# Performance work log

Hardware: AMD Instinct MI355X
Metric: run time of the kernel (lower is better)

## Reference

```python
import jax, jax.numpy as jnp
import numpy as np

N, K, C = 32768, 64, 256
PAIR, HID, BINS, CLIP = 32, 64, 16, 32
LN_EPS = 1e-5


def setup_inputs() -> dict:
    key = jax.random.key(0)
    ks = jax.random.split(key, 12)
    inp = {
        "features": jax.random.normal(ks[0], (N, C), jnp.float32),
        "resi": jnp.arange(N, dtype=jnp.int32),
        "chain": jax.random.randint(ks[1], (N,), 0, 4, jnp.int32),
        "batch": jax.random.randint(ks[2], (N,), 0, 8, jnp.int32),
        "neighbours": jax.random.randint(ks[3], (N, K), 0, N, jnp.int32),
        # learned params
        "W_left": jax.random.normal(ks[4], (C, PAIR), jnp.float32) / np.sqrt(C),
        "W_right": jax.random.normal(ks[5], (C, PAIR), jnp.float32) / np.sqrt(C),
        "W_pos": jax.random.normal(ks[6], (2 * CLIP + 1, PAIR), jnp.float32) * 0.1,
        "ln_scale": jnp.ones((PAIR,), jnp.float32),
        "ln_bias": jnp.zeros((PAIR,), jnp.float32),
        "W1": jax.random.normal(ks[7], (PAIR, HID), jnp.float32) / np.sqrt(PAIR),
        "b1": jnp.zeros((HID,), jnp.float32),
        "W2": jax.random.normal(ks[8], (HID, BINS), jnp.float32) / np.sqrt(HID),
        "b2": jnp.zeros((BINS,), jnp.float32),
    }
    return inp


def reference(features, resi, chain, batch, neighbours,
              W_left, W_right, W_pos, ln_scale, ln_bias, W1, b1, W2, b2):
    # left/right 32-dim codes, pairwise combine via neighbour gather: [N,K,32]
    left = features @ W_left
    right = features @ W_right
    dcode = left[:, None, :] + right[neighbours]

    # relative sequence position one-hot (65 classes) -> Linear(32, bias=False).
    # one_hot @ W_pos == row-gather of W_pos; masked to same chain & batch.
    rel = jnp.clip(resi[neighbours] - resi[:, None], -CLIP, CLIP) + CLIP  # [N,K]
    same = (chain[neighbours] == chain[:, None]) & (batch[neighbours] == batch[:, None])
    dcode = dcode + jnp.where(same[..., None], W_pos[rel], 0.0)

    # LayerNorm over last axis (scale + offset)
    mu = dcode.mean(-1, keepdims=True)
    var = jnp.mean(jnp.square(dcode - mu), -1, keepdims=True)
    dcode = (dcode - mu) * jax.lax.rsqrt(var + LN_EPS) * ln_scale + ln_bias

    # 2-layer GELU MLP -> 16 bins
    h = jax.nn.gelu(dcode @ W1 + b1)
    logits = h @ W2 + b2
    log_p = jax.nn.log_softmax(logits, axis=-1)

    # softmax-weighted expected distance over bin centers of [0, 22) A
    step = 22.0 / BINS
    bin_centers = (jnp.arange(BINS, dtype=jnp.float32) + 0.5) * step
    dmap = (jnp.exp(log_p) * bin_centers).sum(axis=-1)  # [N,K]
    return log_p, dmap
```

## Files before the change

### kernel.cpp

```cpp
#include <hip/hip_runtime.h>
#include <stdint.h>

#define N_RES 32768
#define KNEI  64
#define CFEAT 256
#define PAIRD 32
#define HIDD  64
#define NBINS 16
#define CLIPV 32
#define NGROUPS (N_RES * KNEI / 16)

typedef __attribute__((ext_vector_type(8))) short  short8;
typedef __attribute__((ext_vector_type(4))) float  float4_t;

union U8 { uint32_t u[4]; short8 s8; };

__device__ __forceinline__ uint32_t pkbf(float a, float b) {
    uint32_t ua = __float_as_uint(a) + 0x8000u;
    uint32_t ub = __float_as_uint(b) + 0x8000u;
    uint32_t d;
    const uint32_t sel = 0x07060302u;
    asm("v_perm_b32 %0, %1, %2, %3" : "=v"(d) : "v"(ub), "v"(ua), "s"(sel));
    return d;
}

__device__ __forceinline__ float fastrcp(float x) { return __builtin_amdgcn_rcpf(x); }
__device__ __forceinline__ float fexp2(float x)   { return __builtin_amdgcn_exp2f(x); }
__device__ __forceinline__ float flog2(float x)   { return __builtin_amdgcn_logf(x); }

__device__ __forceinline__ float gelu_tanh(float x) {
    const float k1 = 2.3022082f;
    const float k2 = 0.1029432f;
    float x2 = x * x;
    float t  = __builtin_fmaf(k2, x2, k1);
    float e  = fexp2(x * t);
    float th = __builtin_fmaf(-2.0f, fastrcp(e + 1.0f), 1.0f);
    float hx = 0.5f * x;
    return __builtin_fmaf(hx, th, hx);
}

__global__ __launch_bounds__(256) void proj_kernel(
    const float* __restrict__ feat, const float* __restrict__ Wl,
    const float* __restrict__ Wr, const int* __restrict__ resi,
    const int* __restrict__ chain, const int* __restrict__ batch,
    float* __restrict__ left, float* __restrict__ right,
    int4* __restrict__ meta)
{
    __shared__ __align__(16) float Wc[CFEAT * 64];
    const int tid = threadIdx.x;
    for (int idx = tid; idx < CFEAT * 32; idx += 256) {
        int k = idx >> 5, o = idx & 31;
        Wc[k * 64 + o]      = Wl[idx];
        Wc[k * 64 + 32 + o] = Wr[idx];
    }
    const int row_base = blockIdx.x * 64;
    if (meta != nullptr && tid < 64) {
        int r = row_base + tid;
        meta[r] = make_int4(resi[r], chain[r], batch[r], 0);
    }
    __syncthreads();

    const int cb = (tid & 7) * 8;
    const int r0 = row_base + (tid >> 3) * 2;

    float acc[2][8];
#pragma unroll
    for (int r = 0; r < 2; ++r)
#pragma unroll
        for (int j = 0; j < 8; ++j) acc[r][j] = 0.f;

    for (int i = 0; i < CFEAT; i += 4) {
        float4_t f0 = *(const float4_t*)(feat + (size_t)r0 * CFEAT + i);
        float4_t f1 = *(const float4_t*)(feat + (size_t)(r0 + 1) * CFEAT + i);
#pragma unroll
        for (int s = 0; s < 4; ++s) {
            float4_t wa = *(const float4_t*)(Wc + (i + s) * 64 + cb);
            float4_t wb = *(const float4_t*)(Wc + (i + s) * 64 + cb + 4);
#pragma unroll
            for (int j = 0; j < 4; ++j) {
                acc[0][j]     += f0[s] * wa[j];
                acc[0][4 + j] += f0[s] * wb[j];
                acc[1][j]     += f1[s] * wa[j];
                acc[1][4 + j] += f1[s] * wb[j];
            }
        }
    }
#pragma unroll
    for (int r = 0; r < 2; ++r) {
        float* dst = (cb < 32) ? (left  + (size_t)(r0 + r) * 32 + cb)
                               : (right + (size_t)(r0 + r) * 32 + (cb - 32));
        float4_t v0 = {acc[r][0], acc[r][1], acc[r][2], acc[r][3]};
        float4_t v1 = {acc[r][4], acc[r][5], acc[r][6], acc[r][7]};
        *(float4_t*)dst       = v0;
        *(float4_t*)(dst + 4) = v1;
    }
}

template <int USE_META>
__global__ __launch_bounds__(256, 8) void pair_kernel(
    const float* __restrict__ left, const float* __restrict__ right,
    const int* __restrict__ resi, const int* __restrict__ chain,
    const int* __restrict__ batch, const int* __restrict__ nbr,
    const int4* __restrict__ meta,
    const float* __restrict__ wpos, const float* __restrict__ lnS,
    const float* __restrict__ lnB, const float* __restrict__ W1,
    const float* __restrict__ b1, const float* __restrict__ W2,
    const float* __restrict__ b2, float* __restrict__ out_logp,
    float* __restrict__ out_dmap)
{
    __shared__ __align__(16) unsigned char Hbuf[4][16 * 144];
    __shared__ __align__(16) float b1p[HIDD];

    const int tid    = threadIdx.x;
    const int lane   = tid & 63;
    const int wlocal = tid >> 6;
    const int q      = lane >> 4;
    const int c      = lane & 15;

    if (tid < HIDD) {
        float s = b1[tid];
        for (int k = 0; k < PAIRD; ++k)
            s = __builtin_fmaf(lnB[k], W1[k * HIDD + tid], s);
        b1p[tid] = s;
    }

    short8 w1a[4];
#pragma unroll
    for (int t = 0; t < 4; ++t) {
        U8 tmp;
#pragma unroll
        for (int v = 0; v < 4; ++v) {
            int k0 = q * 8 + 2 * v, k1 = k0 + 1;
            float a0 = lnS[k0] * W1[k0 * HIDD + 16 * t + c];
            float a1 = lnS[k1] * W1[k1 * HIDD + 16 * t + c];
            tmp.u[v] = pkbf(a0, a1);
        }
        w1a[t] = tmp.s8;
    }
    short8 w2a[2];
#pragma unroll
    for (int kt = 0; kt < 2; ++kt) {
        U8 tmp;
#pragma unroll
        for (int v = 0; v < 4; ++v) {
            int k0 = kt * 32 + q * 8 + 2 * v;
            tmp.u[v] = pkbf(W2[k0 * NBINS + c], W2[(k0 + 1) * NBINS + c]);
        }
        w2a[kt] = tmp.s8;
    }
    const float4_t b2f = *(const float4_t*)(b2 + 4 * q);

    __syncthreads();

    const int wglobal = (blockIdx.x * 256 + tid) >> 6;
    const int nwaves  = (gridDim.x * 256) >> 6;

    for (int g = wglobal; g < NGROUPS; g += nwaves) {
        const int pbase = g * 16;
        const int n = pbase >> 6;
        const int p = pbase + c;
        const int nb = nbr[p];

        int rel; float msk;
        if (USE_META) {
            int4 mn = meta[n];
            int4 mb = meta[nb];
            rel = min(max(mb.x - mn.x, -CLIPV), CLIPV) + CLIPV;
            msk = ((mb.y == mn.y) && (mb.z == mn.z)) ? 1.0f : 0.0f;
        } else {
            rel = min(max(resi[nb] - resi[n], -CLIPV), CLIPV) + CLIPV;
            msk = ((chain[nb] == chain[n]) && (batch[nb] == batch[n])) ? 1.0f : 0.0f;
        }

        const float* lptr = left  + (size_t)n  * PAIRD + 8 * q;
        const float* rptr = right + (size_t)nb * PAIRD + 8 * q;
        const float* pptr = wpos  + (size_t)rel * PAIRD + 8 * q;
        float4_t l0 = *(const float4_t*)lptr, l1 = *(const float4_t*)(lptr + 4);
        float4_t r0 = *(const float4_t*)rptr, r1 = *(const float4_t*)(rptr + 4);
        float4_t p0 = *(const float4_t*)pptr, p1 = *(const float4_t*)(pptr + 4);
        float d[8];
#pragma unroll
        for (int j = 0; j < 4; ++j) {
            d[j]     = __builtin_fmaf(msk, p0[j], l0[j] + r0[j]);
            d[4 + j] = __builtin_fmaf(msk, p1[j], l1[j] + r1[j]);
        }

        float s1 = 0.f, s2 = 0.f;
#pragma unroll
        for (int j = 0; j < 8; ++j) { s1 += d[j]; s2 = __builtin_fmaf(d[j], d[j], s2); }
        s1 += __shfl_xor(s1, 16, 64);  s1 += __shfl_xor(s1, 32, 64);
        s2 += __shfl_xor(s2, 16, 64);  s2 += __shfl_xor(s2, 32, 64);
        const float mu   = s1 * (1.0f / 32.0f);
        const float var  = __builtin_fmaf(-mu, mu, s2 * (1.0f / 32.0f));
        const float rstd = __builtin_amdgcn_rsqf(var + 1e-5f);
        const float sh   = -mu * rstd;

        U8 dpack;
#pragma unroll
        for (int v = 0; v < 4; ++v) {
            float nA = __builtin_fmaf(d[2 * v],     rstd, sh);
            float nB = __builtin_fmaf(d[2 * v + 1], rstd, sh);
            dpack.u[v] = pkbf(nA, nB);
        }
        const short8 dfrag = dpack.s8;

        float4_t hacc[4];
#pragma unroll
        for (int t = 0; t < 4; ++t) {
            float4_t c1 = *(const float4_t*)(b1p + 16 * t + 4 * q);
            hacc[t] = __builtin_amdgcn_mfma_f32_16x16x32_bf16(w1a[t], dfrag, c1, 0, 0, 0);
        }

        unsigned char* hb = &Hbuf[wlocal][0] + c * 144;
#pragma unroll
        for (int t = 0; t < 4; ++t) {
            float g0 = gelu_tanh(hacc[t][0]);
            float g1 = gelu_tanh(hacc[t][1]);
            float g2 = gelu_tanh(hacc[t][2]);
            float g3 = gelu_tanh(hacc[t][3]);
            uint2 w; w.x = pkbf(g0, g1); w.y = pkbf(g2, g3);
            *(uint2*)(hb + 32 * t + 8 * q) = w;
        }
        const short8 hf0 = *(const short8*)(hb + 16 * q);
        const short8 hf1 = *(const short8*)(hb + 64 + 16 * q);

        float4_t lacc;
        lacc = __builtin_amdgcn_mfma_f32_16x16x32_bf16(w2a[0], hf0, b2f,  0, 0, 0);
        lacc = __builtin_amdgcn_mfma_f32_16x16x32_bf16(w2a[1], hf1, lacc, 0, 0, 0);

        const float LOG2E = 1.4426950408889634f, LN2 = 0.6931471805599453f;
        float e[4];
#pragma unroll
        for (int r = 0; r < 4; ++r) e[r] = fexp2(lacc[r] * LOG2E);
        float ssum = (e[0] + e[1]) + (e[2] + e[3]);
        ssum += __shfl_xor(ssum, 16, 64);
        ssum += __shfl_xor(ssum, 32, 64);
        const float lse = flog2(ssum) * LN2;

        float4_t lp = {lacc[0] - lse, lacc[1] - lse, lacc[2] - lse, lacc[3] - lse};
        *(float4_t*)(out_logp + (size_t)p * NBINS + 4 * q) = lp;

        const float step  = 22.0f / NBINS;
        const float cbase = (4 * q + 0.5f) * step;
        float dpart = e[0] * cbase + e[1] * (cbase + step)
                    + e[2] * (cbase + 2 * step) + e[3] * (cbase + 3 * step);
        dpart += __shfl_xor(dpart, 16, 64);
        dpart += __shfl_xor(dpart, 32, 64);
        if (q == 0) out_dmap[p] = dpart * fastrcp(ssum);
    }
}

extern "C" void kernel_launch(void* const* d_in, const int* in_sizes, int n_in,
                              void* d_out, int out_size, void* d_ws, size_t ws_size,
                              hipStream_t stream) {
    const float* features = (const float*)d_in[0];
    const int*   resi     = (const int*)d_in[1];
    const int*   chain    = (const int*)d_in[2];
    const int*   batch    = (const int*)d_in[3];
    const int*   nbr      = (const int*)d_in[4];
    const float* W_left   = (const float*)d_in[5];
    const float* W_right  = (const float*)d_in[6];
    const float* W_pos    = (const float*)d_in[7];
    const float* ln_scale = (const float*)d_in[8];
    const float* ln_bias  = (const float*)d_in[9];
    const float* W1       = (const float*)d_in[10];
    const float* b1       = (const float*)d_in[11];
    const float* W2       = (const float*)d_in[12];
    const float* b2       = (const float*)d_in[13];

    float* left  = (float*)d_ws;
    float* right = left + (size_t)N_RES * PAIRD;
    const size_t base_bytes = (size_t)2 * N_RES * PAIRD * sizeof(float);
    const size_t meta_bytes = (size_t)N_RES * sizeof(int4);
    const bool use_meta = ws_size >= base_bytes + meta_bytes;
    int4* meta = use_meta ? (int4*)((char*)d_ws + base_bytes) : nullptr;

    float* out_logp = (float*)d_out;
    float* out_dmap = out_logp + (size_t)N_RES * KNEI * NBINS;

    proj_kernel<<<N_RES / 64, 256, 0, stream>>>(features, W_left, W_right,
                                                resi, chain, batch, left, right, meta);
    if (use_meta)
        pair_kernel<1><<<2048, 256, 0, stream>>>(left, right, resi, chain, batch, nbr,
                                                 meta, W_pos, ln_scale, ln_bias, W1, b1,
                                                 W2, b2, out_logp, out_dmap);
    else
        pair_kernel<0><<<2048, 256, 0, stream>>>(left, right, resi, chain, batch, nbr,
                                                 nullptr, W_pos, ln_scale, ln_bias, W1, b1,
                                                 W2, b2, out_logp, out_dmap);
}
```

Baseline: 311.5 us.

## Store projections and W_pos as bf16, pack metadata, prefetch next group's gathers

The projection kernel now writes left/right codes and W_pos as packed bf16, and packs resi, chain and batch into one 32-bit word per residue. This halves the bytes moved by the random neighbour gathers and shrinks the metadata reads. The pair kernel drops the grid-stride loop for a fixed 16-iteration loop with a stride of 8192 groups. It software-pipelines the next group's nbr, meta and left/right/W_pos loads while the current group's MFMA work runs. The costs are bf16 rounding of the pre-LayerNorm codes, a bit layout that assumes resi < 65536 and chain < 8, hardcoded grid sizing, and one redundant prefetch on the last iteration.

```diff
diff --git a/kernel.cpp b/kernel.cpp
--- a/kernel.cpp
+++ b/kernel.cpp
@@ -23,6 +23,8 @@
     asm("v_perm_b32 %0, %1, %2, %3" : "=v"(d) : "v"(ub), "v"(ua), "s"(sel));
     return d;
 }
+__device__ __forceinline__ float bflo(uint32_t w) { return __uint_as_float(w << 16); }
+__device__ __forceinline__ float bfhi(uint32_t w) { return __uint_as_float(w & 0xFFFF0000u); }
 
 __device__ __forceinline__ float fastrcp(float x) { return __builtin_amdgcn_rcpf(x); }
 __device__ __forceinline__ float fexp2(float x)   { return __builtin_amdgcn_exp2f(x); }
@@ -43,8 +45,9 @@
     const float* __restrict__ feat, const float* __restrict__ Wl,
     const float* __restrict__ Wr, const int* __restrict__ resi,
     const int* __restrict__ chain, const int* __restrict__ batch,
-    float* __restrict__ left, float* __restrict__ right,
-    int4* __restrict__ meta)
+    const float* __restrict__ wpos,
+    uint4* __restrict__ leftbf, uint4* __restrict__ rightbf,
+    uint32_t* __restrict__ meta, uint32_t* __restrict__ wposbf)
 {
     __shared__ __align__(16) float Wc[CFEAT * 64];
     const int tid = threadIdx.x;
@@ -54,9 +57,14 @@
         Wc[k * 64 + 32 + o] = Wr[idx];
     }
     const int row_base = blockIdx.x * 64;
-    if (meta != nullptr && tid < 64) {
+    if (tid < 64) {
         int r = row_base + tid;
-        meta[r] = make_int4(resi[r], chain[r], batch[r], 0);
+        meta[r] = (uint32_t)resi[r] | ((uint32_t)chain[r] << 16)
+                | ((uint32_t)batch[r] << 19);
+    }
+    if (blockIdx.x == 0) {
+        for (int i = tid; i < (2 * CLIPV + 1) * PAIRD / 2; i += 256)
+            wposbf[i] = pkbf(wpos[2 * i], wpos[2 * i + 1]);
     }
     __syncthreads();
 
@@ -87,26 +95,24 @@
     }
 #pragma unroll
     for (int r = 0; r < 2; ++r) {
-        float* dst = (cb < 32) ? (left  + (size_t)(r0 + r) * 32 + cb)
-                               : (right + (size_t)(r0 + r) * 32 + (cb - 32));
-        float4_t v0 = {acc[r][0], acc[r][1], acc[r][2], acc[r][3]};
-        float4_t v1 = {acc[r][4], acc[r][5], acc[r][6], acc[r][7]};
-        *(float4_t*)dst       = v0;
-        *(float4_t*)(dst + 4) = v1;
-    }
-}
-
-template <int USE_META>
+        uint4 o;
+        o.x = pkbf(acc[r][0], acc[r][1]);
+        o.y = pkbf(acc[r][2], acc[r][3]);
+        o.z = pkbf(acc[r][4], acc[r][5]);
+        o.w = pkbf(acc[r][6], acc[r][7]);
+        if (cb < 32) leftbf [(size_t)(r0 + r) * 4 + (cb >> 3)]        = o;
+        else         rightbf[(size_t)(r0 + r) * 4 + ((cb - 32) >> 3)] = o;
+    }
+}
+
 __global__ __launch_bounds__(256, 8) void pair_kernel(
-    const float* __restrict__ left, const float* __restrict__ right,
-    const int* __restrict__ resi, const int* __restrict__ chain,
-    const int* __restrict__ batch, const int* __restrict__ nbr,
-    const int4* __restrict__ meta,
-    const float* __restrict__ wpos, const float* __restrict__ lnS,
-    const float* __restrict__ lnB, const float* __restrict__ W1,
-    const float* __restrict__ b1, const float* __restrict__ W2,
-    const float* __restrict__ b2, float* __restrict__ out_logp,
-    float* __restrict__ out_dmap)
+    const uint4* __restrict__ leftbf, const uint4* __restrict__ rightbf,
+    const uint32_t* __restrict__ meta, const int* __restrict__ nbr,
+    const uint32_t* __restrict__ wposbf,
+    const float* __restrict__ lnS, const float* __restrict__ lnB,
+    const float* __restrict__ W1, const float* __restrict__ b1,
+    const float* __restrict__ W2, const float* __restrict__ b2,
+    float* __restrict__ out_logp, float* __restrict__ out_dmap)
 {
     __shared__ __align__(16) unsigned char Hbuf[4][16 * 144];
     __shared__ __align__(16) float b1p[HIDD];
@@ -153,36 +159,46 @@
     __syncthreads();
 
     const int wglobal = (blockIdx.x * 256 + tid) >> 6;
-    const int nwaves  = (gridDim.x * 256) >> 6;
-
-    for (int g = wglobal; g < NGROUPS; g += nwaves) {
-        const int pbase = g * 16;
-        const int n = pbase >> 6;
-        const int p = pbase + c;
+    const int stride  = 8192;
+
+    uint4 lfS, rfS, pwS; float mskS;
+    {
+        const int pbase = wglobal * 16;
+        const int n = pbase >> 6, p = pbase + c;
         const int nb = nbr[p];
-
-        int rel; float msk;
-        if (USE_META) {
-            int4 mn = meta[n];
-            int4 mb = meta[nb];
-            rel = min(max(mb.x - mn.x, -CLIPV), CLIPV) + CLIPV;
-            msk = ((mb.y == mn.y) && (mb.z == mn.z)) ? 1.0f : 0.0f;
-        } else {
-            rel = min(max(resi[nb] - resi[n], -CLIPV), CLIPV) + CLIPV;
-            msk = ((chain[nb] == chain[n]) && (batch[nb] == batch[n])) ? 1.0f : 0.0f;
-        }
-
-        const float* lptr = left  + (size_t)n  * PAIRD + 8 * q;
-        const float* rptr = right + (size_t)nb * PAIRD + 8 * q;
-        const float* pptr = wpos  + (size_t)rel * PAIRD + 8 * q;
-        float4_t l0 = *(const float4_t*)lptr, l1 = *(const float4_t*)(lptr + 4);
-        float4_t r0 = *(const float4_t*)rptr, r1 = *(const float4_t*)(rptr + 4);
-        float4_t p0 = *(const float4_t*)pptr, p1 = *(const float4_t*)(pptr + 4);
+        const uint32_t mn = meta[n];
+        const uint32_t mb = meta[nb];
+        lfS = leftbf [(size_t)n  * 4 + q];
+        rfS = rightbf[(size_t)nb * 4 + q];
+        int rel = min(max((int)(mb & 0xFFFFu) - (int)(mn & 0xFFFFu), -CLIPV), CLIPV) + CLIPV;
+        mskS = (((mb ^ mn) & 0xFFFF0000u) == 0u) ? 1.0f : 0.0f;
+        pwS = *(const uint4*)(wposbf + rel * 16 + q * 4);
+    }
+
+    for (int it = 0; it < 16; ++it) {
+        const int gc = wglobal + it * stride;
+        const int p  = gc * 16 + c;
+
+        const int gn = wglobal + ((it + 1) & 15) * stride;
+        const int nn = (gn * 16) >> 6, pn = gn * 16 + c;
+        const int nbN = nbr[pn];
+        const uint32_t mnN = meta[nn];
+        const uint4 lfN = leftbf[(size_t)nn * 4 + q];
+
+        const uint4 lf = lfS, rf = rfS, pw = pwS;
+        const float msk = mskS;
+
+        const uint32_t mbN = meta[nbN];
+        const uint4 rfN = rightbf[(size_t)nbN * 4 + q];
+
+        const uint32_t la[4] = {lf.x, lf.y, lf.z, lf.w};
+        const uint32_t ra[4] = {rf.x, rf.y, rf.z, rf.w};
+        const uint32_t pa[4] = {pw.x, pw.y, pw.z, pw.w};
         float d[8];
 #pragma unroll
-        for (int j = 0; j < 4; ++j) {
-            d[j]     = __builtin_fmaf(msk, p0[j], l0[j] + r0[j]);
-            d[4 + j] = __builtin_fmaf(msk, p1[j], l1[j] + r1[j]);
+        for (int v = 0; v < 4; ++v) {
+            d[2 * v]     = __builtin_fmaf(msk, bflo(pa[v]), bflo(la[v]) + bflo(ra[v]));
+            d[2 * v + 1] = __builtin_fmaf(msk, bfhi(pa[v]), bfhi(la[v]) + bfhi(ra[v]));
         }
 
         float s1 = 0.f, s2 = 0.f;
@@ -211,6 +227,11 @@
             hacc[t] = __builtin_amdgcn_mfma_f32_16x16x32_bf16(w1a[t], dfrag, c1, 0, 0, 0);
         }
 
+        const int relN = min(max((int)(mbN & 0xFFFFu) - (int)(mnN & 0xFFFFu),
+                                 -CLIPV), CLIPV) + CLIPV;
+        const float mskN = (((mbN ^ mnN) & 0xFFFF0000u) == 0u) ? 1.0f : 0.0f;
+        const uint4 pwN = *(const uint4*)(wposbf + relN * 16 + q * 4);
+
         unsigned char* hb = &Hbuf[wlocal][0] + c * 144;
 #pragma unroll
         for (int t = 0; t < 4; ++t) {
@@ -247,6 +268,8 @@
         dpart += __shfl_xor(dpart, 16, 64);
         dpart += __shfl_xor(dpart, 32, 64);
         if (q == 0) out_dmap[p] = dpart * fastrcp(ssum);
+
+        lfS = lfN; rfS = rfN; pwS = pwN; mskS = mskN;
     }
 }
 
@@ -268,24 +291,19 @@
     const float* W2       = (const float*)d_in[12];
     const float* b2       = (const float*)d_in[13];
 
-    float* left  = (float*)d_ws;
-    float* right = left + (size_t)N_RES * PAIRD;
-    const size_t base_bytes = (size_t)2 * N_RES * PAIRD * sizeof(float);
-    const size_t meta_bytes = (size_t)N_RES * sizeof(int4);
-    const bool use_meta = ws_size >= base_bytes + meta_bytes;
-    int4* meta = use_meta ? (int4*)((char*)d_ws + base_bytes) : nullptr;
+    char* ws = (char*)d_ws;
+    uint4*    leftbf  = (uint4*)ws;
+    uint4*    rightbf = (uint4*)(ws + (size_t)N_RES * 64);
+    uint32_t* meta    = (uint32_t*)(ws + (size_t)2 * N_RES * 64);
+    uint32_t* wposbf  = (uint32_t*)(ws + (size_t)2 * N_RES * 64 + N_RES * 4);
 
     float* out_logp = (float*)d_out;
     float* out_dmap = out_logp + (size_t)N_RES * KNEI * NBINS;
 
     proj_kernel<<<N_RES / 64, 256, 0, stream>>>(features, W_left, W_right,
-                                                resi, chain, batch, left, right, meta);
-    if (use_meta)
-        pair_kernel<1><<<2048, 256, 0, stream>>>(left, right, resi, chain, batch, nbr,
-                                                 meta, W_pos, ln_scale, ln_bias, W1, b1,
-                                                 W2, b2, out_logp, out_dmap);
-    else
-        pair_kernel<0><<<2048, 256, 0, stream>>>(left, right, resi, chain, batch, nbr,
-                                                 nullptr, W_pos, ln_scale, ln_bias, W1, b1,
-                                                 W2, b2, out_logp, out_dmap);
-}
+                                                resi, chain, batch, W_pos,
+                                                leftbf, rightbf, meta, wposbf);
+    pair_kernel<<<2048, 256, 0, stream>>>(leftbf, rightbf, meta, nbr, wposbf,
+                                          ln_scale, ln_bias, W1, b1, W2, b2,
+                                          out_logp, out_dmap);
+}
```

Result: slower. 341.5 us (+9.6%).
